# Optimization experiments

Measured on AMD Instinct MI355X. Metric: run time of the kernel, lower is better.

Reference implementation:

```python
import jax, jax.numpy as jnp
import numpy as np

B, C, H, W = 64, 512, 64, 64
RED = 16
HID = C // RED  # 32
N_EXPERTS = 3

def setup_inputs() -> dict:
    key = jax.random.key(0)
    k1, k2, k3, k4 = jax.random.split(key, 4)
    x = jax.random.normal(k1, (B, C, H, W), dtype=jnp.float32)
    dataset = jax.random.randint(k2, (B,), 0, N_EXPERTS, dtype=jnp.int32)
    # torch Linear weight layout: [out_features, in_features]
    W1 = jax.random.normal(k3, (N_EXPERTS, HID, C), dtype=jnp.float32) * (1.0 / np.sqrt(C))
    W2 = jax.random.normal(k4, (N_EXPERTS, C, HID), dtype=jnp.float32) * (1.0 / np.sqrt(HID))
    return {"x": x, "dataset": dataset, "W1": W1, "W2": W2}

def reference(x, dataset, W1, W2):
    # global average pool: [B, C]
    y = jnp.mean(x, axis=(2, 3))
    # per-sample expert weights, routed by dataset id
    w1 = W1[dataset]  # [B, HID, C]
    w2 = W2[dataset]  # [B, C, HID]
    h = jax.nn.relu(jnp.einsum('bc,bhc->bh', y, w1))
    gate = jax.nn.sigmoid(jnp.einsum('bh,bch->bc', h, w2))  # [B, C]
    return x * gate[:, :, None, None]
```

## Files before the change

kernel.cpp:

```cpp
#include <hip/hip_runtime.h>
#include <math.h>

#define NB 64
#define NC 512
#define NHW 4096
#define NHID 32
#define NPLANES (NB * NC)

typedef float f32x4 __attribute__((ext_vector_type(4)));

__global__ __launch_bounds__(256) void pool_kernel(const float* __restrict__ x,
                                                   float* __restrict__ y) {
    const int wid   = threadIdx.x >> 6;
    const int lane  = threadIdx.x & 63;
    const int plane = blockIdx.x * 4 + wid;
    const f32x4* __restrict__ xin =
        reinterpret_cast<const f32x4*>(x + (size_t)plane * NHW);

    float s = 0.f;
#pragma unroll
    for (int i = 0; i < 16; ++i) {
        f32x4 v = xin[lane + i * 64];
        s += v.x + v.y + v.z + v.w;
    }
#pragma unroll
    for (int o = 32; o; o >>= 1) s += __shfl_down(s, o, 64);
    if (lane == 0) y[plane] = s * (1.0f / NHW);
}

__global__ __launch_bounds__(256) void gate_kernel(const float* __restrict__ y,
                                                   const int* __restrict__ dataset,
                                                   const float* __restrict__ W1,
                                                   const float* __restrict__ W2,
                                                   float* __restrict__ gate) {
    const int b = blockIdx.x;
    const int tid = threadIdx.x;

    __shared__ float ys[NC];
    __shared__ float hs[NHID];

    ys[tid]       = y[b * NC + tid];
    ys[tid + 256] = y[b * NC + tid + 256];
    const int e = dataset[b];
    __syncthreads();

    const int hid = tid >> 3;
    const int j   = tid & 7;
    const float* __restrict__ w1row = W1 + ((size_t)e * NHID + hid) * NC;
    float acc = 0.f;
    for (int c = j; c < NC; c += 8) acc += ys[c] * w1row[c];
#pragma unroll
    for (int o = 4; o; o >>= 1) acc += __shfl_down(acc, o, 8);
    if (j == 0) hs[hid] = fmaxf(acc, 0.f);
    __syncthreads();

    const float* __restrict__ w2base = W2 + (size_t)e * NC * NHID;
#pragma unroll
    for (int k = 0; k < 2; ++k) {
        const int c = tid + k * 256;
        const float* __restrict__ w2row = w2base + c * NHID;
        float z = 0.f;
#pragma unroll
        for (int hh = 0; hh < NHID; ++hh) z += hs[hh] * w2row[hh];
        gate[b * NC + c] = 1.0f / (1.0f + expf(-z));
    }
}

__global__ __launch_bounds__(256) void scale_kernel(const float* __restrict__ x,
                                                    const float* __restrict__ gate,
                                                    float* __restrict__ out) {
    const int pair = (NPLANES / 2 - 1) - blockIdx.x;
    const int p0 = pair * 2;
    const float g0 = gate[p0];
    const float g1 = gate[p0 + 1];
    const size_t base = (size_t)pair * 2048;
    const f32x4* __restrict__ xin = reinterpret_cast<const f32x4*>(x);
    f32x4* __restrict__ o4 = reinterpret_cast<f32x4*>(out);
    const int t = threadIdx.x;

#pragma unroll
    for (int k = 0; k < 4; ++k) {
        const size_t i = base + (size_t)k * 256 + t;
        f32x4 v = xin[i];
        v *= g0;
        __builtin_nontemporal_store(v, &o4[i]);
    }
#pragma unroll
    for (int k = 0; k < 4; ++k) {
        const size_t i = base + 1024 + (size_t)k * 256 + t;
        f32x4 v = xin[i];
        v *= g1;
        __builtin_nontemporal_store(v, &o4[i]);
    }
}

extern "C" void kernel_launch(void* const* d_in, const int* in_sizes, int n_in,
                              void* d_out, int out_size, void* d_ws, size_t ws_size,
                              hipStream_t stream) {
    const float* x       = (const float*)d_in[0];
    const int*   dataset = (const int*)d_in[1];
    const float* W1      = (const float*)d_in[2];
    const float* W2      = (const float*)d_in[3];
    float* out = (float*)d_out;

    float* y    = (float*)d_ws;
    float* gate = y + NB * NC;

    pool_kernel<<<NPLANES / 4, 256, 0, stream>>>(x, y);
    gate_kernel<<<NB, 256, 0, stream>>>(y, dataset, W1, W2, gate);
    scale_kernel<<<NPLANES / 2, 256, 0, stream>>>(x, gate, out);
}
```

Measured before the change: 284.9 us.

## Chunk batch into pool/gate/scale passes so scale rereads x from cache

Splits the batch into four chunks of sixteen samples and runs the pool, gate and scale kernels per chunk. Each chunk's input slice is small enough to stay resident in the last-level cache, so the scale pass can reread x from cache instead of HBM. The trade-off is more kernel launches, less parallelism per launch, and serialization at chunk boundaries, and it drops the earlier reverse-order scale trick.

```diff
diff --git a/kernel.cpp b/kernel.cpp
--- a/kernel.cpp
+++ b/kernel.cpp
@@ -6,14 +6,17 @@
 #define NHW 4096
 #define NHID 32
 #define NPLANES (NB * NC)
+#define CHB 16
+#define NCHUNK (NB / CHB)
+#define CHPLANES (CHB * NC)
 
 typedef float f32x4 __attribute__((ext_vector_type(4)));
 
 __global__ __launch_bounds__(256) void pool_kernel(const float* __restrict__ x,
-                                                   float* __restrict__ y) {
+                                                   float* __restrict__ y, int p0) {
     const int wid   = threadIdx.x >> 6;
     const int lane  = threadIdx.x & 63;
-    const int plane = blockIdx.x * 4 + wid;
+    const int plane = p0 + blockIdx.x * 4 + wid;
     const f32x4* __restrict__ xin =
         reinterpret_cast<const f32x4*>(x + (size_t)plane * NHW);
 
@@ -32,8 +35,8 @@
                                                    const int* __restrict__ dataset,
                                                    const float* __restrict__ W1,
                                                    const float* __restrict__ W2,
-                                                   float* __restrict__ gate) {
-    const int b = blockIdx.x;
+                                                   float* __restrict__ gate, int b0) {
+    const int b = b0 + blockIdx.x;
     const int tid = threadIdx.x;
 
     __shared__ float ys[NC];
@@ -68,11 +71,11 @@
 
 __global__ __launch_bounds__(256) void scale_kernel(const float* __restrict__ x,
                                                     const float* __restrict__ gate,
-                                                    float* __restrict__ out) {
-    const int pair = (NPLANES / 2 - 1) - blockIdx.x;
-    const int p0 = pair * 2;
-    const float g0 = gate[p0];
-    const float g1 = gate[p0 + 1];
+                                                    float* __restrict__ out, int p0) {
+    const int pair = p0 / 2 + blockIdx.x;
+    const int pl0 = pair * 2;
+    const float g0 = gate[pl0];
+    const float g1 = gate[pl0 + 1];
     const size_t base = (size_t)pair * 2048;
     const f32x4* __restrict__ xin = reinterpret_cast<const f32x4*>(x);
     f32x4* __restrict__ o4 = reinterpret_cast<f32x4*>(out);
@@ -106,7 +109,11 @@
     float* y    = (float*)d_ws;
     float* gate = y + NB * NC;
 
-    pool_kernel<<<NPLANES / 4, 256, 0, stream>>>(x, y);
-    gate_kernel<<<NB, 256, 0, stream>>>(y, dataset, W1, W2, gate);
-    scale_kernel<<<NPLANES / 2, 256, 0, stream>>>(x, gate, out);
+    for (int c = 0; c < NCHUNK; ++c) {
+        const int b0 = c * CHB;
+        const int p0 = b0 * NC;
+        pool_kernel <<<CHPLANES / 4, 256, 0, stream>>>(x, y, p0);
+        gate_kernel <<<CHB,          256, 0, stream>>>(y, dataset, W1, W2, gate, b0);
+        scale_kernel<<<CHPLANES / 2, 256, 0, stream>>>(x, gate, out, p0);
+    }
 }
```

Result: slower. 308.8 us (+8.4%).
